# Kernel tuning notes

Measured on AMD Instinct MI355X. Metric: run time of the kernel, lower is better.

Reference implementation:

```python
import jax, jax.numpy as jnp
import numpy as np

H = 8      # heads
D = 64     # dim_head
DIM = 512  # model dim (== H*D)
LN_EPS = 1e-5


def setup_inputs() -> dict:
    key = jax.random.key(0)
    ks = jax.random.split(key, 4)
    B, N = 8, 1024
    x = jax.random.normal(ks[0], (B, N, DIM), dtype=jnp.float32)
    # params (torch Linear y = x @ W^T; we store W already transposed as (in, out))
    w_qkv = jax.random.normal(ks[1], (DIM, 3 * H * D), dtype=jnp.float32) * (DIM ** -0.5)
    w_out = jax.random.normal(ks[2], (H * D, DIM), dtype=jnp.float32) * ((H * D) ** -0.5)
    b_out = jnp.zeros((DIM,), dtype=jnp.float32)
    ln_g = jnp.ones((DIM,), dtype=jnp.float32)
    ln_b = jnp.zeros((DIM,), dtype=jnp.float32)
    return {"x": x, "w_qkv": w_qkv, "w_out": w_out, "b_out": b_out,
            "ln_g": ln_g, "ln_b": ln_b}


def reference(x, w_qkv, w_out, b_out, ln_g, ln_b):
    b, n, _ = x.shape
    qkv = x @ w_qkv                                   # [b, n, 3*H*D]
    q, k, v = jnp.split(qkv, 3, axis=-1)              # each [b, n, H*D]

    def to_heads(t):                                  # 'b n (h d) -> (b h) n d'
        return t.reshape(b, n, H, D).transpose(0, 2, 1, 3).reshape(b * H, n, D)

    q = to_heads(q)
    k = to_heads(k)
    v = to_heads(v)

    # FAITHFUL to source: k.view(b*h, -1, n) is a row-major reshape, NOT a
    # transpose, and NO scale is applied (self.scale is unused in forward).
    k_r = k.reshape(b * H, D, n)                      # [(bh), D, n] reinterpreted
    dots = jnp.matmul(q, k_r)                          # [(bh), n, n]
    attn = jax.nn.softmax(dots, axis=-1)
    out = jnp.matmul(attn, v)                          # [(bh), n, D]

    # '(b h) n d -> b n (h d)'
    out = out.reshape(b, H, n, D).transpose(0, 2, 1, 3).reshape(b, n, H * D)
    out = out @ w_out + b_out                          # to_out Linear (dropout=0)

    mu = jnp.mean(out, axis=-1, keepdims=True)
    var = jnp.var(out, axis=-1, keepdims=True)
    out = (out - mu) * jax.lax.rsqrt(var + LN_EPS) * ln_g + ln_b
    return out + x
```

## Files before the change

kernel.cpp:

```cpp
#include <hip/hip_runtime.h>

typedef unsigned short u16;
typedef unsigned int u32;
typedef __attribute__((ext_vector_type(4))) float f32x4;
typedef __attribute__((ext_vector_type(8))) short s16x8;

__device__ __forceinline__ u16 bf16_rne(float f) {
    u32 u = __float_as_uint(f);
    u32 r = u + 0x7FFFu + ((u >> 16) & 1u);
    return (u16)(r >> 16);
}

__device__ __forceinline__ u32 cvt_pk_bf16(float lo, float hi) {
    u32 r;
    asm("v_cvt_pk_bf16_f32 %0, %1, %2" : "=v"(r) : "v"(lo), "v"(hi));
    return r;
}

__device__ __forceinline__ void gl_lds16(const void* g, void* l) {
    __builtin_amdgcn_global_load_lds(
        (const __attribute__((address_space(1))) u32*)g,
        (__attribute__((address_space(3))) u32*)l, 16, 0, 0);
}

#define MFMA16(a, b, c) __builtin_amdgcn_mfma_f32_16x16x32_bf16((a), (b), (c), 0, 0, 0)

__global__ __launch_bounds__(256) void k_convert(const float* __restrict__ in,
                                                 u16* __restrict__ out, int n4) {
    int i = blockIdx.x * 256 + threadIdx.x;
    if (i >= n4) return;
    f32x4 v = *(const f32x4*)(in + (size_t)i * 4);
    u32 lo = (u32)bf16_rne(v.x) | ((u32)bf16_rne(v.y) << 16);
    u32 hi = (u32)bf16_rne(v.z) | ((u32)bf16_rne(v.w) << 16);
    u32* p = (u32*)(out + (size_t)i * 4);
    p[0] = lo;
    p[1] = hi;
}

__global__ __launch_bounds__(256) void k_transpose_bf16(const float* __restrict__ in,
                                                        u16* __restrict__ out,
                                                        int R, int C) {
    __shared__ float tile[32][33];
    int bx = blockIdx.x * 32;
    int by = blockIdx.y * 32;
    int tx = threadIdx.x;
    int ty = threadIdx.y;
#pragma unroll
    for (int i = 0; i < 32; i += 8)
        tile[ty + i][tx] = in[(size_t)(by + ty + i) * C + bx + tx];
    __syncthreads();
#pragma unroll
    for (int i = 0; i < 32; i += 8)
        out[(size_t)(bx + ty + i) * R + by + tx] = bf16_rne(tile[tx][ty + i]);
}

__global__ __launch_bounds__(256) void k_qkv_gemm(
    const u16* __restrict__ xbf, const u16* __restrict__ wt,
    u16* __restrict__ qh, u16* __restrict__ kRT, u16* __restrict__ vT) {
    __shared__ __align__(16) u16 lA[2][128 * 64];
    __shared__ __align__(16) u16 lB[2][128 * 64];
    const int tid = threadIdx.x;
    const int lane = tid & 63, l15 = lane & 15, l4 = lane >> 4;
    const int wid = tid >> 6, wm = wid >> 1, wn = wid & 1;
    const int m0 = blockIdx.y * 128;
    const int c0 = blockIdx.x * 128;

    const char* gA = (const char*)xbf + (size_t)m0 * 1024;
    const char* gB = (const char*)wt + (size_t)c0 * 1024;
    const int srow = tid >> 3;
    const int scol = (tid & 7) * 16;

    const f32x4 z4 = {0.f, 0.f, 0.f, 0.f};
    f32x4 acc[4][4];
#pragma unroll
    for (int i = 0; i < 4; ++i)
#pragma unroll
        for (int j = 0; j < 4; ++j) acc[i][j] = z4;

    auto stage = [&](int buf, int kt) {
#pragma unroll
        for (int q = 0; q < 4; ++q) {
            int row = q * 32 + srow;
            int sc = scol ^ ((row & 7) << 4);
            gl_lds16(gA + (size_t)row * 1024 + kt * 128 + sc,
                     (char*)lA[buf] + q * 4096 + tid * 16);
            gl_lds16(gB + (size_t)row * 1024 + kt * 128 + sc,
                     (char*)lB[buf] + q * 4096 + tid * 16);
        }
    };

    stage(0, 0);
    __syncthreads();
    for (int kt = 0; kt < 8; ++kt) {
        int buf = kt & 1;
        if (kt < 7) stage(buf ^ 1, kt + 1);
        s16x8 af[4][2], bfr[4][2];
#pragma unroll
        for (int i = 0; i < 4; ++i)
#pragma unroll
            for (int k2 = 0; k2 < 2; ++k2) {
                int ra = wm * 64 + i * 16 + l15;
                int ca = (k2 * 64 + l4 * 16) ^ ((ra & 7) << 4);
                af[i][k2] = *(const s16x8*)((const char*)lA[buf] + ra * 128 + ca);
                int rb = wn * 64 + i * 16 + l15;
                int cb = (k2 * 64 + l4 * 16) ^ ((rb & 7) << 4);
                bfr[i][k2] = *(const s16x8*)((const char*)lB[buf] + rb * 128 + cb);
            }
#pragma unroll
        for (int i = 0; i < 4; ++i)
#pragma unroll
            for (int j = 0; j < 4; ++j)
#pragma unroll
                for (int k2 = 0; k2 < 2; ++k2)
                    acc[i][j] = MFMA16(af[i][k2], bfr[j][k2], acc[i][j]);
        __syncthreads();
    }

    char* ct = (char*)lA;
    const int which = c0 >> 9;
    const int hb = (c0 & 511) >> 6;
    const int b = m0 >> 10;
    const int n0 = m0 & 1023;
    const int i4 = (m0 >> 7) & 7;

    if (which != 2) {
#pragma unroll
        for (int i = 0; i < 4; ++i)
#pragma unroll
            for (int j = 0; j < 4; ++j) {
                int col = wn * 64 + j * 16 + l15;
#pragma unroll
                for (int r = 0; r < 4; ++r) {
                    int rr = wm * 64 + i * 16 + l4 * 4 + r;
                    *(u16*)(ct + rr * 256 + ((col * 2) ^ ((rr & 7) << 4))) =
                        bf16_rne(acc[i][j][r]);
                }
            }
    } else {
#pragma unroll
        for (int i = 0; i < 4; ++i)
#pragma unroll
            for (int j = 0; j < 4; ++j) {
                int col = wn * 64 + j * 16 + l15;
#pragma unroll
                for (int r = 0; r < 4; ++r) {
                    int rr = wm * 64 + i * 16 + l4 * 4 + r;
                    *(u16*)(ct + col * 256 + ((rr * 2) ^ ((col & 7) << 4))) =
                        bf16_rne(acc[i][j][r]);
                }
            }
    }
    __syncthreads();

    if (which == 0) {
#pragma unroll
        for (int p = 0; p < 8; ++p) {
            int cid = p * 256 + tid;
            int row = cid >> 4, sub = cid & 15;
            s16x8 v = *(const s16x8*)(ct + row * 256 + ((sub * 16) ^ ((row & 7) << 4)));
            int bh = b * 8 + hb + (sub >> 3);
            *(s16x8*)((char*)qh + ((size_t)bh * 1024 + n0 + row) * 128 +
                      (sub & 7) * 16) = v;
        }
    } else if (which == 1) {
#pragma unroll
        for (int p = 0; p < 8; ++p) {
            int cid = p * 256 + tid;
            int h = cid >> 10, jb = (cid >> 6) & 15, jd = cid & 63;
            int colb = ((h * 64 + jd) * 2) ^ ((jb & 7) << 4);
            s16x8 v;
#pragma unroll
            for (int ii = 0; ii < 8; ++ii)
                v[ii] = *(const short*)(ct + (jb + ii * 16) * 256 + colb);
            int bh = b * 8 + hb + h;
            *(s16x8*)((char*)kRT + (size_t)bh * 131072 + jb * 8192 + i4 * 1024 +
                      jd * 16) = v;
        }
    } else {
#pragma unroll
        for (int p = 0; p < 8; ++p) {
            int cid = p * 256 + tid;
            int cl = cid >> 4, nc = cid & 15;
            s16x8 v = *(const s16x8*)(ct + cl * 256 + ((nc * 16) ^ ((cl & 7) << 4)));
            int bh = b * 8 + hb + (cl >> 6);
            *(s16x8*)((char*)vT + ((size_t)bh * 64 + (cl & 63)) * 2048 + n0 * 2 +
                      nc * 16) = v;
        }
    }
}

__global__ __launch_bounds__(512) void k_attn(
    const u16* __restrict__ qh, const u16* __restrict__ kRT,
    const u16* __restrict__ vT, u16* __restrict__ attn_out) {
    __shared__ __align__(16) char smem[49152];
    char* qtile = smem;
    char* ktb = smem + 16384;
    char* vtb = smem + 32768;

    const int tid = threadIdx.x;
    const int lane = tid & 63, l15 = lane & 15, l4 = lane >> 4;
    const int wid = tid >> 6;
    const int bh = blockIdx.x, mt = blockIdx.y;

    const char* kb = (const char*)kRT + (size_t)bh * 131072;
    const char* vb = (const char*)vT + (size_t)bh * 64 * 2048;
    const int srow = tid >> 3;
    const int scol = (tid & 7) * 16;

    {
        const char* gq = (const char*)qh + ((size_t)bh * 1024 + mt * 128) * 128;
#pragma unroll
        for (int q = 0; q < 2; ++q) {
            int row = q * 64 + srow;
            int sc = scol ^ ((row & 7) << 4);
            gl_lds16(gq + (size_t)row * 128 + sc, qtile + q * 8192 + tid * 16);
        }
        int i4s = (tid & 7) ^ (srow & 7);
        gl_lds16(kb + i4s * 1024 + srow * 16, ktb + tid * 16);
        int sc = scol ^ ((srow & 7) << 4);
        gl_lds16(vb + (size_t)srow * 2048 + sc, vtb + tid * 16);
    }
    __syncthreads();

    s16x8 qf[2];
#pragma unroll
    for (int k2 = 0; k2 < 2; ++k2) {
        int row = wid * 16 + l15;
        int cq = (k2 * 64 + l4 * 16) ^ ((row & 7) << 4);
        qf[k2] = *(const s16x8*)(qtile + row * 128 + cq);
    }
    __syncthreads();

    char* ptw = smem + wid * 2048;

    const f32x4 z4 = {0.f, 0.f, 0.f, 0.f};
    f32x4 o[4];
    float den = 0.f;
#pragma unroll
    for (int d4 = 0; d4 < 4; ++d4) o[d4] = z4;
    const float LOG2E = 1.4426950408889634f;

    for (int jb = 0; jb < 16; ++jb) {
        const int buf = jb & 1;
        if (jb < 15) {
            int nb = jb + 1, bufn = buf ^ 1;
            int i4s = (tid & 7) ^ (srow & 7);
            gl_lds16(kb + (size_t)nb * 8192 + i4s * 1024 + srow * 16,
                     ktb + bufn * 8192 + tid * 16);
            int sc = scol ^ ((srow & 7) << 4);
            gl_lds16(vb + (size_t)srow * 2048 + nb * 128 + sc,
                     vtb + bufn * 8192 + tid * 16);
        }
        const char* kt = ktb + buf * 8192;
        const char* vt = vtb + buf * 8192;

        s16x8 bk[4][2];
#pragma unroll
        for (int n4 = 0; n4 < 4; ++n4)
#pragma unroll
            for (int k2 = 0; k2 < 2; ++k2) {
                int rn = n4 * 16 + l15;
                int cb = (k2 * 64 + l4 * 16) ^ ((rn & 7) << 4);
                bk[n4][k2] = *(const s16x8*)(kt + rn * 128 + cb);
            }
        f32x4 s[4];
        __builtin_amdgcn_s_setprio(1);
#pragma unroll
        for (int n4 = 0; n4 < 4; ++n4) {
            s[n4] = z4;
#pragma unroll
            for (int k2 = 0; k2 < 2; ++k2)
                s[n4] = MFMA16(bk[n4][k2], qf[k2], s[n4]);
        }
        __builtin_amdgcn_s_setprio(0);

#pragma unroll
        for (int n4 = 0; n4 < 4; ++n4) {
            float e0 = exp2f(s[n4][0] * LOG2E);
            float e1 = exp2f(s[n4][1] * LOG2E);
            float e2 = exp2f(s[n4][2] * LOG2E);
            float e3 = exp2f(s[n4][3] * LOG2E);
            den += (e0 + e1) + (e2 + e3);
            uint2 w;
            w.x = cvt_pk_bf16(e0, e1);
            w.y = cvt_pk_bf16(e2, e3);
            *(uint2*)(ptw + l15 * 128 +
                      ((n4 * 32 + l4 * 8) ^ ((l15 & 7) << 4))) = w;
        }

        s16x8 bv[4][2];
#pragma unroll
        for (int d4 = 0; d4 < 4; ++d4)
#pragma unroll
            for (int k2 = 0; k2 < 2; ++k2) {
                int rn = d4 * 16 + l15;
                int cb = (k2 * 64 + l4 * 16) ^ ((rn & 7) << 4);
                bv[d4][k2] = *(const s16x8*)(vt + rn * 128 + cb);
            }

        s16x8 pa[2];
#pragma unroll
        for (int k2 = 0; k2 < 2; ++k2)
            pa[k2] = *(const s16x8*)(ptw + l15 * 128 +
                                     ((k2 * 64 + l4 * 16) ^ ((l15 & 7) << 4)));

        __builtin_amdgcn_s_setprio(1);
#pragma unroll
        for (int d4 = 0; d4 < 4; ++d4)
#pragma unroll
            for (int k2 = 0; k2 < 2; ++k2)
                o[d4] = MFMA16(bv[d4][k2], pa[k2], o[d4]);
        __builtin_amdgcn_s_setprio(0);

        if (jb < 15) __syncthreads();
    }

    den += __shfl_xor(den, 16);
    den += __shfl_xor(den, 32);
    float inv = 1.0f / den;

    {
        int row = wid * 16 + l15;
        char* ow = smem + row * 128;
#pragma unroll
        for (int d4 = 0; d4 < 4; ++d4) {
            uint2 w;
            w.x = cvt_pk_bf16(o[d4][0] * inv, o[d4][1] * inv);
            w.y = cvt_pk_bf16(o[d4][2] * inv, o[d4][3] * inv);
            *(uint2*)(ow + ((d4 * 32 + l4 * 8) ^ ((row & 7) << 4))) = w;
        }
    }
    __syncthreads();

    {
        char* dst = (char*)attn_out + ((size_t)(bh >> 3) * 1024 + mt * 128) * 1024 +
                    (bh & 7) * 128;
#pragma unroll
        for (int p = 0; p < 2; ++p) {
            int cid = p * 512 + tid;
            int row = cid >> 3, sub = cid & 7;
            s16x8 v = *(const s16x8*)(smem + row * 128 +
                                      ((sub * 16) ^ ((row & 7) << 4)));
            *(s16x8*)(dst + (size_t)row * 1024 + sub * 16) = v;
        }
    }
}

__global__ __launch_bounds__(256) void k_out_gemm(
    const u16* __restrict__ a, const u16* __restrict__ wt,
    const float* __restrict__ bias, float* __restrict__ proj) {
    __shared__ __align__(16) char smem[65536];
    u16* lA[2] = {(u16*)smem, (u16*)(smem + 16384)};
    u16* lB[2] = {(u16*)(smem + 32768), (u16*)(smem + 49152)};
    const int tid = threadIdx.x;
    const int lane = tid & 63, l15 = lane & 15, l4 = lane >> 4;
    const int wid = tid >> 6, wm = wid >> 1, wn = wid & 1;
    const int m0 = blockIdx.y * 128;
    const int c0 = blockIdx.x * 128;

    const char* gA = (const char*)a + (size_t)m0 * 1024;
    const char* gB = (const char*)wt + (size_t)c0 * 1024;
    const int srow = tid >> 3;
    const int scol = (tid & 7) * 16;

    const f32x4 z4 = {0.f, 0.f, 0.f, 0.f};
    f32x4 acc[4][4];
#pragma unroll
    for (int i = 0; i < 4; ++i)
#pragma unroll
        for (int j = 0; j < 4; ++j) acc[i][j] = z4;

    auto stage = [&](int buf, int kt) {
#pragma unroll
        for (int q = 0; q < 4; ++q) {
            int row = q * 32 + srow;
            int sc = scol ^ ((row & 7) << 4);
            gl_lds16(gA + (size_t)row * 1024 + kt * 128 + sc,
                     (char*)lA[buf] + q * 4096 + tid * 16);
            gl_lds16(gB + (size_t)row * 1024 + kt * 128 + sc,
                     (char*)lB[buf] + q * 4096 + tid * 16);
        }
    };

    stage(0, 0);
    __syncthreads();
    for (int kt = 0; kt < 8; ++kt) {
        int buf = kt & 1;
        if (kt < 7) stage(buf ^ 1, kt + 1);
        s16x8 af[4][2], bfr[4][2];
#pragma unroll
        for (int i = 0; i < 4; ++i)
#pragma unroll
            for (int k2 = 0; k2 < 2; ++k2) {
                int ra = wm * 64 + i * 16 + l15;
                int ca = (k2 * 64 + l4 * 16) ^ ((ra & 7) << 4);
                af[i][k2] = *(const s16x8*)((const char*)lA[buf] + ra * 128 + ca);
                int rb = wn * 64 + i * 16 + l15;
                int cb = (k2 * 64 + l4 * 16) ^ ((rb & 7) << 4);
                bfr[i][k2] = *(const s16x8*)((const char*)lB[buf] + rb * 128 + cb);
            }
#pragma unroll
        for (int i = 0; i < 4; ++i)
#pragma unroll
            for (int j = 0; j < 4; ++j)
#pragma unroll
                for (int k2 = 0; k2 < 2; ++k2)
                    acc[i][j] = MFMA16(af[i][k2], bfr[j][k2], acc[i][j]);
        __syncthreads();
    }

#pragma unroll
    for (int i = 0; i < 4; ++i)
#pragma unroll
        for (int j = 0; j < 4; ++j) {
            int col = wn * 64 + j * 16 + l15;
            float bo = bias[c0 + col];
#pragma unroll
            for (int r = 0; r < 4; ++r) {
                int rr = wm * 64 + i * 16 + l4 * 4 + r;
                *(float*)(smem + rr * 512 + ((col * 4) ^ ((rr & 7) << 4))) =
                    acc[i][j][r] + bo;
            }
        }
    __syncthreads();
#pragma unroll
    for (int p = 0; p < 16; ++p) {
        int cid = p * 256 + tid;
        int row = cid >> 5, sub = cid & 31;
        f32x4 v = *(const f32x4*)(smem + row * 512 + ((sub * 16) ^ ((row & 7) << 4)));
        *(f32x4*)((char*)proj + (size_t)(m0 + row) * 2048 + c0 * 4 + sub * 16) = v;
    }
}

__global__ __launch_bounds__(256) void k_ln(const float* __restrict__ proj,
                                            const float* __restrict__ x,
                                            const float* __restrict__ g,
                                            const float* __restrict__ bb,
                                            float* __restrict__ out) {
    const int lane = threadIdx.x & 63, wid = threadIdx.x >> 6;
    const int row = blockIdx.x * 4 + wid;
    const float* pr = proj + (size_t)row * 512;
    f32x4 v0 = *(const f32x4*)(pr + lane * 4);
    f32x4 v1 = *(const f32x4*)(pr + 256 + lane * 4);
    float s = v0.x + v0.y + v0.z + v0.w + v1.x + v1.y + v1.z + v1.w;
    float sq = v0.x * v0.x + v0.y * v0.y + v0.z * v0.z + v0.w * v0.w +
               v1.x * v1.x + v1.y * v1.y + v1.z * v1.z + v1.w * v1.w;
#pragma unroll
    for (int m = 1; m < 64; m <<= 1) {
        s += __shfl_xor(s, m);
        sq += __shfl_xor(sq, m);
    }
    float mu = s * (1.0f / 512.0f);
    float var = sq * (1.0f / 512.0f) - mu * mu;
    float rstd = rsqrtf(var + 1e-5f);

    const float* xr = x + (size_t)row * 512;
    f32x4 x0 = *(const f32x4*)(xr + lane * 4);
    f32x4 x1 = *(const f32x4*)(xr + 256 + lane * 4);
    f32x4 g0 = *(const f32x4*)(g + lane * 4);
    f32x4 g1 = *(const f32x4*)(g + 256 + lane * 4);
    f32x4 b0 = *(const f32x4*)(bb + lane * 4);
    f32x4 b1 = *(const f32x4*)(bb + 256 + lane * 4);
    f32x4 r0, r1;
#pragma unroll
    for (int u = 0; u < 4; ++u) {
        r0[u] = (v0[u] - mu) * rstd * g0[u] + b0[u] + x0[u];
        r1[u] = (v1[u] - mu) * rstd * g1[u] + b1[u] + x1[u];
    }
    float* orow = out + (size_t)row * 512;
    *(f32x4*)(orow + lane * 4) = r0;
    *(f32x4*)(orow + 256 + lane * 4) = r1;
}

extern "C" void kernel_launch(void* const* d_in, const int* in_sizes, int n_in,
                              void* d_out, int out_size, void* d_ws, size_t ws_size,
                              hipStream_t stream) {
    const float* x = (const float*)d_in[0];
    const float* w_qkv = (const float*)d_in[1];
    const float* w_out = (const float*)d_in[2];
    const float* b_out = (const float*)d_in[3];
    const float* ln_g = (const float*)d_in[4];
    const float* ln_b = (const float*)d_in[5];
    float* out = (float*)d_out;
    char* ws = (char*)d_ws;

    u16* xbf = (u16*)(ws + 0);
    u16* wqkvt = (u16*)(ws + 8388608);
    u16* woutt = (u16*)(ws + 9961472);
    u16* qh = (u16*)(ws + 10485760);
    u16* kRT = (u16*)(ws + 18874368);
    u16* vT = (u16*)(ws + 27262976);
    u16* aout = (u16*)(ws + 35651584);
    float* proj = (float*)(ws + 10485760);

    k_convert<<<4096, 256, 0, stream>>>(x, xbf, 1048576);
    k_transpose_bf16<<<dim3(48, 16), dim3(32, 8), 0, stream>>>(w_qkv, wqkvt, 512, 1536);
    k_transpose_bf16<<<dim3(16, 16), dim3(32, 8), 0, stream>>>(w_out, woutt, 512, 512);
    k_qkv_gemm<<<dim3(12, 64), 256, 0, stream>>>(xbf, wqkvt, qh, kRT, vT);
    k_attn<<<dim3(64, 8), 512, 0, stream>>>(qh, kRT, vT, aout);
    k_out_gemm<<<dim3(4, 64), 256, 0, stream>>>(aout, woutt, b_out, proj);
    k_ln<<<2048, 256, 0, stream>>>(proj, x, ln_g, ln_b, out);
}
```

Baseline: 84.99 us.

## Fuse x conversion into QKV GEMM, out-proj with LayerNorm, merge weight transposes

The QKV GEMM now loads fp32 x directly, converts it to bf16 in registers and writes it to LDS, which removes the separate convert kernel and its bf16 round trip. The output projection is fused with the LayerNorm and residual in one 512-thread kernel that computes full 32x512 row tiles, so the fp32 proj buffer is never written or re-read. The two weight transposes are merged into one launch, and s_setprio hints are wrapped around the MFMA loops. In exchange, the x loads are now register-staged instead of async global-to-LDS copies, and the fused kernel uses 128KB of LDS with only 256 blocks, which may limit occupancy.

```diff
diff --git a/kernel.cpp b/kernel.cpp
--- a/kernel.cpp
+++ b/kernel.cpp
@@ -4,6 +4,7 @@
 typedef unsigned int u32;
 typedef __attribute__((ext_vector_type(4))) float f32x4;
 typedef __attribute__((ext_vector_type(8))) short s16x8;
+typedef __attribute__((ext_vector_type(4))) unsigned int u32x4;
 
 __device__ __forceinline__ u16 bf16_rne(float f) {
     u32 u = __float_as_uint(f);
@@ -25,23 +26,18 @@
 
 #define MFMA16(a, b, c) __builtin_amdgcn_mfma_f32_16x16x32_bf16((a), (b), (c), 0, 0, 0)
 
-__global__ __launch_bounds__(256) void k_convert(const float* __restrict__ in,
-                                                 u16* __restrict__ out, int n4) {
-    int i = blockIdx.x * 256 + threadIdx.x;
-    if (i >= n4) return;
-    f32x4 v = *(const f32x4*)(in + (size_t)i * 4);
-    u32 lo = (u32)bf16_rne(v.x) | ((u32)bf16_rne(v.y) << 16);
-    u32 hi = (u32)bf16_rne(v.z) | ((u32)bf16_rne(v.w) << 16);
-    u32* p = (u32*)(out + (size_t)i * 4);
-    p[0] = lo;
-    p[1] = hi;
-}
-
-__global__ __launch_bounds__(256) void k_transpose_bf16(const float* __restrict__ in,
-                                                        u16* __restrict__ out,
-                                                        int R, int C) {
+__global__ __launch_bounds__(256) void k_transpose2(const float* __restrict__ w_qkv,
+                                                    const float* __restrict__ w_out,
+                                                    u16* __restrict__ wqkvt,
+                                                    u16* __restrict__ woutt) {
     __shared__ float tile[32][33];
-    int bx = blockIdx.x * 32;
+    const float* in;
+    u16* out;
+    int C, bxc;
+    if (blockIdx.x < 48) { in = w_qkv; out = wqkvt; C = 1536; bxc = blockIdx.x; }
+    else                 { in = w_out; out = woutt; C = 512;  bxc = blockIdx.x - 48; }
+    const int R = 512;
+    int bx = bxc * 32;
     int by = blockIdx.y * 32;
     int tx = threadIdx.x;
     int ty = threadIdx.y;
@@ -55,7 +51,7 @@
 }
 
 __global__ __launch_bounds__(256) void k_qkv_gemm(
-    const u16* __restrict__ xbf, const u16* __restrict__ wt,
+    const float* __restrict__ x, const u16* __restrict__ wt,
     u16* __restrict__ qh, u16* __restrict__ kRT, u16* __restrict__ vT) {
     __shared__ __align__(16) u16 lA[2][128 * 64];
     __shared__ __align__(16) u16 lB[2][128 * 64];
@@ -65,10 +61,11 @@
     const int m0 = blockIdx.y * 128;
     const int c0 = blockIdx.x * 128;
 
-    const char* gA = (const char*)xbf + (size_t)m0 * 1024;
+    const char* gX = (const char*)x + (size_t)m0 * 2048;
     const char* gB = (const char*)wt + (size_t)c0 * 1024;
     const int srow = tid >> 3;
-    const int scol = (tid & 7) * 16;
+    const int cc = tid & 7;
+    const int scol = cc * 16;
 
     const f32x4 z4 = {0.f, 0.f, 0.f, 0.f};
     f32x4 acc[4][4];
@@ -77,23 +74,47 @@
 #pragma unroll
         for (int j = 0; j < 4; ++j) acc[i][j] = z4;
 
-    auto stage = [&](int buf, int kt) {
+    f32x4 ax[4][2];
+    auto loadA = [&](int kt) {
+#pragma unroll
+        for (int q = 0; q < 4; ++q) {
+            const char* src = gX + (size_t)(q * 32 + srow) * 2048 + kt * 256 + cc * 32;
+            ax[q][0] = *(const f32x4*)(src);
+            ax[q][1] = *(const f32x4*)(src + 16);
+        }
+    };
+    auto writeA = [&](int buf) {
+#pragma unroll
+        for (int q = 0; q < 4; ++q) {
+            int row = q * 32 + srow;
+            u32x4 v;
+            v.x = cvt_pk_bf16(ax[q][0].x, ax[q][0].y);
+            v.y = cvt_pk_bf16(ax[q][0].z, ax[q][0].w);
+            v.z = cvt_pk_bf16(ax[q][1].x, ax[q][1].y);
+            v.w = cvt_pk_bf16(ax[q][1].z, ax[q][1].w);
+            *(u32x4*)((char*)lA[buf] + row * 128 + (scol ^ ((row & 7) << 4))) = v;
+        }
+    };
+    auto stageB = [&](int buf, int kt) {
 #pragma unroll
         for (int q = 0; q < 4; ++q) {
             int row = q * 32 + srow;
             int sc = scol ^ ((row & 7) << 4);
-            gl_lds16(gA + (size_t)row * 1024 + kt * 128 + sc,
-                     (char*)lA[buf] + q * 4096 + tid * 16);
             gl_lds16(gB + (size_t)row * 1024 + kt * 128 + sc,
                      (char*)lB[buf] + q * 4096 + tid * 16);
         }
     };
 
-    stage(0, 0);
+    loadA(0);
+    stageB(0, 0);
+    writeA(0);
     __syncthreads();
     for (int kt = 0; kt < 8; ++kt) {
         int buf = kt & 1;
-        if (kt < 7) stage(buf ^ 1, kt + 1);
+        if (kt < 7) {
+            loadA(kt + 1);
+            stageB(buf ^ 1, kt + 1);
+        }
         s16x8 af[4][2], bfr[4][2];
 #pragma unroll
         for (int i = 0; i < 4; ++i)
@@ -106,6 +127,7 @@
                 int cb = (k2 * 64 + l4 * 16) ^ ((rb & 7) << 4);
                 bfr[i][k2] = *(const s16x8*)((const char*)lB[buf] + rb * 128 + cb);
             }
+        __builtin_amdgcn_s_setprio(1);
 #pragma unroll
         for (int i = 0; i < 4; ++i)
 #pragma unroll
@@ -113,6 +135,8 @@
 #pragma unroll
                 for (int k2 = 0; k2 < 2; ++k2)
                     acc[i][j] = MFMA16(af[i][k2], bfr[j][k2], acc[i][j]);
+        __builtin_amdgcn_s_setprio(0);
+        if (kt < 7) writeA(buf ^ 1);
         __syncthreads();
     }
 
@@ -346,130 +370,114 @@
     }
 }
 
-__global__ __launch_bounds__(256) void k_out_gemm(
-    const u16* __restrict__ a, const u16* __restrict__ wt,
-    const float* __restrict__ bias, float* __restrict__ proj) {
-    __shared__ __align__(16) char smem[65536];
-    u16* lA[2] = {(u16*)smem, (u16*)(smem + 16384)};
-    u16* lB[2] = {(u16*)(smem + 32768), (u16*)(smem + 49152)};
+__global__ __launch_bounds__(512) void k_out_ln(
+    const u16* __restrict__ aout, const u16* __restrict__ wt,
+    const float* __restrict__ bias, const float* __restrict__ x,
+    const float* __restrict__ g, const float* __restrict__ bb,
+    float* __restrict__ out) {
+    __shared__ __align__(16) char smem[131072];
+    char* lB[2] = {smem, smem + 65536};
     const int tid = threadIdx.x;
     const int lane = tid & 63, l15 = lane & 15, l4 = lane >> 4;
-    const int wid = tid >> 6, wm = wid >> 1, wn = wid & 1;
-    const int m0 = blockIdx.y * 128;
-    const int c0 = blockIdx.x * 128;
-
-    const char* gA = (const char*)a + (size_t)m0 * 1024;
-    const char* gB = (const char*)wt + (size_t)c0 * 1024;
-    const int srow = tid >> 3;
-    const int scol = (tid & 7) * 16;
+    const int wid = tid >> 6, wm = wid >> 2, wn = wid & 3;
+    const int m0 = blockIdx.x * 32;
+
+    s16x8 af[16];
+    {
+        const char* arow = (const char*)aout + (size_t)(m0 + wm * 16 + l15) * 1024;
+#pragma unroll
+        for (int kk = 0; kk < 16; ++kk)
+            af[kk] = *(const s16x8*)(arow + kk * 64 + l4 * 16);
+    }
+
+    auto stageB = [&](int buf, int kt) {
+#pragma unroll
+        for (int p = 0; p < 8; ++p) {
+            int cid = p * 512 + tid;
+            int n = cid >> 3, cc = cid & 7;
+            int sc = (cc * 16) ^ ((n & 7) << 4);
+            gl_lds16((const char*)wt + (size_t)n * 1024 + kt * 128 + sc,
+                     lB[buf] + cid * 16);
+        }
+    };
 
     const f32x4 z4 = {0.f, 0.f, 0.f, 0.f};
-    f32x4 acc[4][4];
-#pragma unroll
-    for (int i = 0; i < 4; ++i)
-#pragma unroll
-        for (int j = 0; j < 4; ++j) acc[i][j] = z4;
-
-    auto stage = [&](int buf, int kt) {
-#pragma unroll
-        for (int q = 0; q < 4; ++q) {
-            int row = q * 32 + srow;
-            int sc = scol ^ ((row & 7) << 4);
-            gl_lds16(gA + (size_t)row * 1024 + kt * 128 + sc,
-                     (char*)lA[buf] + q * 4096 + tid * 16);
-            gl_lds16(gB + (size_t)row * 1024 + kt * 128 + sc,
-                     (char*)lB[buf] + q * 4096 + tid * 16);
-        }
-    };
-
-    stage(0, 0);
+    f32x4 acc[8];
+#pragma unroll
+    for (int j = 0; j < 8; ++j) acc[j] = z4;
+
+    stageB(0, 0);
     __syncthreads();
     for (int kt = 0; kt < 8; ++kt) {
         int buf = kt & 1;
-        if (kt < 7) stage(buf ^ 1, kt + 1);
-        s16x8 af[4][2], bfr[4][2];
-#pragma unroll
-        for (int i = 0; i < 4; ++i)
-#pragma unroll
-            for (int k2 = 0; k2 < 2; ++k2) {
-                int ra = wm * 64 + i * 16 + l15;
-                int ca = (k2 * 64 + l4 * 16) ^ ((ra & 7) << 4);
-                af[i][k2] = *(const s16x8*)((const char*)lA[buf] + ra * 128 + ca);
-                int rb = wn * 64 + i * 16 + l15;
-                int cb = (k2 * 64 + l4 * 16) ^ ((rb & 7) << 4);
-                bfr[i][k2] = *(const s16x8*)((const char*)lB[buf] + rb * 128 + cb);
+        if (kt < 7) stageB(buf ^ 1, kt + 1);
+        s16x8 bf2[8][2];
+#pragma unroll
+        for (int j = 0; j < 8; ++j)
+#pragma unroll
+            for (int q = 0; q < 2; ++q) {
+                int n = wn * 128 + j * 16 + l15;
+                int cb = (q * 64 + l4 * 16) ^ ((n & 7) << 4);
+                bf2[j][q] = *(const s16x8*)(lB[buf] + n * 128 + cb);
             }
-#pragma unroll
-        for (int i = 0; i < 4; ++i)
-#pragma unroll
-            for (int j = 0; j < 4; ++j)
-#pragma unroll
-                for (int k2 = 0; k2 < 2; ++k2)
-                    acc[i][j] = MFMA16(af[i][k2], bfr[j][k2], acc[i][j]);
+        __builtin_amdgcn_s_setprio(1);
+#pragma unroll
+        for (int j = 0; j < 8; ++j)
+#pragma unroll
+            for (int q = 0; q < 2; ++q)
+                acc[j] = MFMA16(af[kt * 2 + q], bf2[j][q], acc[j]);
+        __builtin_amdgcn_s_setprio(0);
         __syncthreads();
     }
 
 #pragma unroll
-    for (int i = 0; i < 4; ++i)
-#pragma unroll
-        for (int j = 0; j < 4; ++j) {
-            int col = wn * 64 + j * 16 + l15;
-            float bo = bias[c0 + col];
-#pragma unroll
-            for (int r = 0; r < 4; ++r) {
-                int rr = wm * 64 + i * 16 + l4 * 4 + r;
-                *(float*)(smem + rr * 512 + ((col * 4) ^ ((rr & 7) << 4))) =
-                    acc[i][j][r] + bo;
-            }
-        }
-    __syncthreads();
-#pragma unroll
-    for (int p = 0; p < 16; ++p) {
-        int cid = p * 256 + tid;
-        int row = cid >> 5, sub = cid & 31;
-        f32x4 v = *(const f32x4*)(smem + row * 512 + ((sub * 16) ^ ((row & 7) << 4)));
-        *(f32x4*)((char*)proj + (size_t)(m0 + row) * 2048 + c0 * 4 + sub * 16) = v;
-    }
-}
-
-__global__ __launch_bounds__(256) void k_ln(const float* __restrict__ proj,
-                                            const float* __restrict__ x,
-                                            const float* __restrict__ g,
-                                            const float* __restrict__ bb,
-                                            float* __restrict__ out) {
-    const int lane = threadIdx.x & 63, wid = threadIdx.x >> 6;
-    const int row = blockIdx.x * 4 + wid;
-    const float* pr = proj + (size_t)row * 512;
-    f32x4 v0 = *(const f32x4*)(pr + lane * 4);
-    f32x4 v1 = *(const f32x4*)(pr + 256 + lane * 4);
-    float s = v0.x + v0.y + v0.z + v0.w + v1.x + v1.y + v1.z + v1.w;
-    float sq = v0.x * v0.x + v0.y * v0.y + v0.z * v0.z + v0.w * v0.w +
-               v1.x * v1.x + v1.y * v1.y + v1.z * v1.z + v1.w * v1.w;
-#pragma unroll
-    for (int m = 1; m < 64; m <<= 1) {
-        s += __shfl_xor(s, m);
-        sq += __shfl_xor(sq, m);
-    }
-    float mu = s * (1.0f / 512.0f);
-    float var = sq * (1.0f / 512.0f) - mu * mu;
-    float rstd = rsqrtf(var + 1e-5f);
-
-    const float* xr = x + (size_t)row * 512;
-    f32x4 x0 = *(const f32x4*)(xr + lane * 4);
-    f32x4 x1 = *(const f32x4*)(xr + 256 + lane * 4);
-    f32x4 g0 = *(const f32x4*)(g + lane * 4);
-    f32x4 g1 = *(const f32x4*)(g + 256 + lane * 4);
-    f32x4 b0 = *(const f32x4*)(bb + lane * 4);
-    f32x4 b1 = *(const f32x4*)(bb + 256 + lane * 4);
-    f32x4 r0, r1;
-#pragma unroll
-    for (int u = 0; u < 4; ++u) {
-        r0[u] = (v0[u] - mu) * rstd * g0[u] + b0[u] + x0[u];
-        r1[u] = (v1[u] - mu) * rstd * g1[u] + b1[u] + x1[u];
-    }
-    float* orow = out + (size_t)row * 512;
-    *(f32x4*)(orow + lane * 4) = r0;
-    *(f32x4*)(orow + 256 + lane * 4) = r1;
+    for (int j = 0; j < 8; ++j) {
+        int col = wn * 128 + j * 16 + l15;
+        float bo = bias[col];
+#pragma unroll
+        for (int r = 0; r < 4; ++r) {
+            int row = wm * 16 + l4 * 4 + r;
+            *(float*)(smem + row * 2048 + ((col * 4) ^ ((row & 7) << 4))) =
+                acc[j][r] + bo;
+        }
+    }
+    __syncthreads();
+
+    f32x4 g0 = *(const f32x4*)(g + lane * 8);
+    f32x4 g1 = *(const f32x4*)(g + lane * 8 + 4);
+    f32x4 b0 = *(const f32x4*)(bb + lane * 8);
+    f32x4 b1 = *(const f32x4*)(bb + lane * 8 + 4);
+#pragma unroll
+    for (int rr = 0; rr < 4; ++rr) {
+        int row = wid * 4 + rr;
+        int sw = (row & 7) << 4;
+        f32x4 v0 = *(const f32x4*)(smem + row * 2048 + ((lane * 32) ^ sw));
+        f32x4 v1 = *(const f32x4*)(smem + row * 2048 + ((lane * 32 + 16) ^ sw));
+        float s = v0.x + v0.y + v0.z + v0.w + v1.x + v1.y + v1.z + v1.w;
+        float sq = v0.x * v0.x + v0.y * v0.y + v0.z * v0.z + v0.w * v0.w +
+                   v1.x * v1.x + v1.y * v1.y + v1.z * v1.z + v1.w * v1.w;
+#pragma unroll
+        for (int m = 1; m < 64; m <<= 1) {
+            s += __shfl_xor(s, m);
+            sq += __shfl_xor(sq, m);
+        }
+        float mu = s * (1.0f / 512.0f);
+        float var = sq * (1.0f / 512.0f) - mu * mu;
+        float rstd = rsqrtf(var + 1e-5f);
+
+        const float* xr = x + (size_t)(m0 + row) * 512 + lane * 8;
+        f32x4 x0 = *(const f32x4*)(xr);
+        f32x4 x1 = *(const f32x4*)(xr + 4);
+        f32x4 r0, r1;
+#pragma unroll
+        for (int u = 0; u < 4; ++u) {
+            r0[u] = (v0[u] - mu) * rstd * g0[u] + b0[u] + x0[u];
+            r1[u] = (v1[u] - mu) * rstd * g1[u] + b1[u] + x1[u];
+        }
+        float* orow = out + (size_t)(m0 + row) * 512 + lane * 8;
+        *(f32x4*)(orow) = r0;
+        *(f32x4*)(orow + 4) = r1;
+    }
 }
 
 extern "C" void kernel_launch(void* const* d_in, const int* in_sizes, int n_in,
@@ -484,20 +492,15 @@
     float* out = (float*)d_out;
     char* ws = (char*)d_ws;
 
-    u16* xbf = (u16*)(ws + 0);
-    u16* wqkvt = (u16*)(ws + 8388608);
-    u16* woutt = (u16*)(ws + 9961472);
-    u16* qh = (u16*)(ws + 10485760);
-    u16* kRT = (u16*)(ws + 18874368);
-    u16* vT = (u16*)(ws + 27262976);
-    u16* aout = (u16*)(ws + 35651584);
-    float* proj = (float*)(ws + 10485760);
-
-    k_convert<<<4096, 256, 0, stream>>>(x, xbf, 1048576);
-    k_transpose_bf16<<<dim3(48, 16), dim3(32, 8), 0, stream>>>(w_qkv, wqkvt, 512, 1536);
-    k_transpose_bf16<<<dim3(16, 16), dim3(32, 8), 0, stream>>>(w_out, woutt, 512, 512);
-    k_qkv_gemm<<<dim3(12, 64), 256, 0, stream>>>(xbf, wqkvt, qh, kRT, vT);
+    u16* wqkvt = (u16*)(ws + 0);
+    u16* woutt = (u16*)(ws + 1572864);
+    u16* qh = (u16*)(ws + 2097152);
+    u16* kRT = (u16*)(ws + 10485760);
+    u16* vT = (u16*)(ws + 18874368);
+    u16* aout = (u16*)(ws + 27262976);
+
+    k_transpose2<<<dim3(64, 16), dim3(32, 8), 0, stream>>>(w_qkv, w_out, wqkvt, woutt);
+    k_qkv_gemm<<<dim3(12, 64), 256, 0, stream>>>(x, wqkvt, qh, kRT, vT);
     k_attn<<<dim3(64, 8), 512, 0, stream>>>(qh, kRT, vT, aout);
-    k_out_gemm<<<dim3(4, 64), 256, 0, stream>>>(aout, woutt, b_out, proj);
-    k_ln<<<2048, 256, 0, stream>>>(proj, x, ln_g, ln_b, out);
-}
+    k_out_ln<<<256, 512, 0, stream>>>(aout, woutt, b_out, x, ln_g, ln_b, out);
+}
```

New measurement: 87.46 us. 1.03x slower.
